# Kernel tuning notes

Measured on AMD Instinct MI355X. Metric: run time of the kernel, lower is better.

## Reference

```python
import jax, jax.numpy as jnp
import numpy as np

B, S, N_STATE, N_HEAD = 2, 2048, 1024, 16
HEAD_DIM = N_STATE // N_HEAD


def setup_inputs() -> dict:
    key = jax.random.key(0)
    ks = jax.random.split(key, 9)
    w_scale = N_STATE ** -0.5
    x = jax.random.normal(ks[0], (B, S, N_STATE), jnp.float32)
    # Whisper-style additive causal mask with -inf above the diagonal
    mask = jnp.triu(jnp.full((S, S), -jnp.inf, jnp.float32), k=1)
    Wq = jax.random.normal(ks[1], (N_STATE, N_STATE), jnp.float32) * w_scale
    bq = jax.random.normal(ks[2], (N_STATE,), jnp.float32) * 0.01
    Wk = jax.random.normal(ks[3], (N_STATE, N_STATE), jnp.float32) * w_scale  # no bias
    Wv = jax.random.normal(ks[4], (N_STATE, N_STATE), jnp.float32) * w_scale
    bv = jax.random.normal(ks[5], (N_STATE,), jnp.float32) * 0.01
    Wo = jax.random.normal(ks[6], (N_STATE, N_STATE), jnp.float32) * w_scale
    bo = jax.random.normal(ks[7], (N_STATE,), jnp.float32) * 0.01
    return {"x": x, "mask": mask, "Wq": Wq, "bq": bq, "Wk": Wk,
            "Wv": Wv, "bv": bv, "Wo": Wo, "bo": bo}


def reference(x, mask, Wq, bq, Wk, Wv, bv, Wo, bo):
    b, s, n_state = x.shape
    scale = (n_state // N_HEAD) ** -0.25
    q = (x @ Wq + bq).reshape(b, s, N_HEAD, HEAD_DIM)  # [b,s,h,d]
    k = (x @ Wk).reshape(b, s, N_HEAD, HEAD_DIM)
    v = (x @ Wv + bv).reshape(b, s, N_HEAD, HEAD_DIM)
    # scale applied to both q and k as in source
    qk = jnp.einsum('bqhd,bkhd->bhqk', q * scale, k * scale)
    qk = qk + mask[:s, :s]
    qk = qk.astype(jnp.float32)
    qk = jnp.where(jnp.isinf(qk), -1e9, qk)
    w = jax.nn.softmax(qk, axis=-1).astype(q.dtype)  # [b,h,q,k]
    wv = jnp.einsum('bhqk,bkhd->bqhd', w, v).reshape(b, s, n_state)
    out = wv @ Wo + bo
    return (out, qk)
```

## Files before the change

kernel.cpp:

```cpp
#include <hip/hip_runtime.h>

typedef __attribute__((ext_vector_type(8))) short short8;
typedef __attribute__((ext_vector_type(4))) float f32x4;

#define SEQ   2048
#define NST   1024
#define NHD   16
#define HDM   64
#define BSZ   2
#define MTOT  (BSZ*SEQ)

__device__ __forceinline__ unsigned short f2bf(float f) {
    union { float f; unsigned int u; } v; v.f = f;
    return (unsigned short)((v.u + 0x7fffu + ((v.u >> 16) & 1u)) >> 16);
}

__device__ __forceinline__ void gload_lds16(const void* g, void* l) {
    __builtin_amdgcn_global_load_lds((const __attribute__((address_space(1))) void*)g,
                                     (__attribute__((address_space(3))) void*)l, 16, 0, 0);
}

__global__ void k_convert(const float* __restrict__ x, unsigned short* __restrict__ out, int n) {
    int i = (blockIdx.x * 256 + threadIdx.x) * 8;
    if (i >= n) return;
    float4 a = *(const float4*)(x + i);
    float4 b = *(const float4*)(x + i + 4);
    short8 v;
    v[0] = (short)f2bf(a.x); v[1] = (short)f2bf(a.y);
    v[2] = (short)f2bf(a.z); v[3] = (short)f2bf(a.w);
    v[4] = (short)f2bf(b.x); v[5] = (short)f2bf(b.y);
    v[6] = (short)f2bf(b.z); v[7] = (short)f2bf(b.w);
    *(short8*)(out + i) = v;
}

__global__ void k_transpose_bf16(const float* __restrict__ W, unsigned short* __restrict__ Wt) {
    __shared__ float t[32][33];
    int n0 = blockIdx.x * 32, k0 = blockIdx.y * 32;
    int c = threadIdx.x & 31, rr = threadIdx.x >> 5;
    for (int i = 0; i < 4; i++) {
        int r = i * 8 + rr;
        t[r][c] = W[(k0 + r) * NST + n0 + c];
    }
    __syncthreads();
    for (int i = 0; i < 4; i++) {
        int r = i * 8 + rr;
        Wt[(n0 + r) * NST + k0 + c] = f2bf(t[c][r]);
    }
}

__global__ void k_vt(const unsigned short* __restrict__ v, unsigned short* __restrict__ vt) {
    __shared__ unsigned short t[64 * 72];
    int jt = blockIdx.x, bh = blockIdx.y;
    int b = bh >> 4, h = bh & 15;
    int tid = threadIdx.x;
    for (int i = 0; i < 2; i++) {
        int id = i * 256 + tid;
        int row = id >> 3, dc = (id & 7) * 8;
        *(short8*)(t + row * 72 + dc) =
            *(const short8*)(v + ((size_t)(b * SEQ + jt * 64 + row)) * NST + h * HDM + dc);
    }
    __syncthreads();
    for (int i = 0; i < 2; i++) {
        int id = i * 256 + tid;
        int d = id >> 3, jc = (id & 7) * 8;
        short8 vv;
        for (int u = 0; u < 8; u++) vv[u] = (short)t[(jc + u) * 72 + d];
        *(short8*)(vt + ((size_t)(bh * HDM + d)) * SEQ + jt * 64 + jc) = vv;
    }
}

template<bool OUT_BF16>
__global__ __launch_bounds__(256) void k_gemm(const unsigned short* __restrict__ A,
                                              const unsigned short* __restrict__ Bt,
                                              const float* __restrict__ bias, float scale,
                                              void* __restrict__ outp) {
    __shared__ __align__(16) unsigned short As[128 * 32];
    __shared__ __align__(16) unsigned short Bs[64 * 32];
    int m0 = blockIdx.y * 128, n0 = blockIdx.x * 64;
    int tid = threadIdx.x, lane = tid & 63, wave = tid >> 6;
    int quad = lane >> 4, l16 = lane & 15;
    int wm = (wave & 1) * 64, wn = (wave >> 1) * 32;
    int p = lane & 3;
    int sz = (quad ^ ((l16 >> 1) & 3)) * 8;
    f32x4 acc[4][2] = {};
    for (int k0 = 0; k0 < NST; k0 += 32) {
        __syncthreads();
        for (int j = 0; j < 2; j++) {
            int row = wave * 32 + j * 16 + (lane >> 2);
            int qb = (p ^ ((row >> 1) & 3)) * 8;
            gload_lds16(A + (size_t)(m0 + row) * NST + k0 + qb, As + (wave * 32 + j * 16) * 32);
        }
        {
            int row = wave * 16 + (lane >> 2);
            int qb = (p ^ ((row >> 1) & 3)) * 8;
            gload_lds16(Bt + (size_t)(n0 + row) * NST + k0 + qb, Bs + wave * 16 * 32);
        }
        __syncthreads();
        short8 a[4], b[2];
        for (int mi = 0; mi < 4; mi++)
            a[mi] = *(const short8*)(As + (wm + mi * 16 + l16) * 32 + sz);
        for (int ni = 0; ni < 2; ni++)
            b[ni] = *(const short8*)(Bs + (wn + ni * 16 + l16) * 32 + sz);
        for (int mi = 0; mi < 4; mi++)
            for (int ni = 0; ni < 2; ni++)
                acc[mi][ni] = __builtin_amdgcn_mfma_f32_16x16x32_bf16(a[mi], b[ni], acc[mi][ni], 0, 0, 0);
    }
    for (int ni = 0; ni < 2; ni++) {
        int col = n0 + wn + ni * 16 + l16;
        float bv = bias ? bias[col] : 0.0f;
        for (int mi = 0; mi < 4; mi++) {
            for (int r = 0; r < 4; r++) {
                int row = m0 + wm + mi * 16 + quad * 4 + r;
                float val = (acc[mi][ni][r] + bv) * scale;
                if (OUT_BF16) ((unsigned short*)outp)[row * NST + col] = f2bf(val);
                else          ((float*)outp)[row * NST + col] = val;
            }
        }
    }
}

__global__ void k_fill_upper(float* __restrict__ qk) {
    int jt = blockIdx.x, qt = blockIdx.y, bh = blockIdx.z;
    if (jt <= qt) return;
    float4 val = make_float4(-1e9f, -1e9f, -1e9f, -1e9f);
    for (int i = 0; i < 4; i++) {
        int lin = i * 256 + threadIdx.x;
        int row = lin >> 4, c4 = (lin & 15) * 4;
        *(float4*)(qk + ((size_t)bh * SEQ + qt * 64 + row) * SEQ + jt * 64 + c4) = val;
    }
}

__global__ __launch_bounds__(256) void k_attn(const unsigned short* __restrict__ qb,
                                              const unsigned short* __restrict__ kb,
                                              const unsigned short* __restrict__ vtg,
                                              float* __restrict__ qk,
                                              unsigned short* __restrict__ wv) {
    __shared__ __align__(16) unsigned short Ks[64 * 64];
    __shared__ __align__(16) unsigned short Vs[64 * 64];
    __shared__ __align__(16) unsigned short Plds[4 * 16 * 72];
    int pair = blockIdx.x, bh = blockIdx.y;
    int b = bh >> 4, h = bh & 15;
    int tid = threadIdx.x, lane = tid & 63, wave = tid >> 6;
    int quad = lane >> 4, l16 = lane & 15;
    unsigned short* pbuf = Plds + wave * 16 * 72;
    int srow = lane >> 3;
    int spb = lane & 7;
    short o1 = (short)0x3F80;
    short8 vones = {o1, o1, o1, o1, o1, o1, o1, o1};
    int fx0 = (quad ^ (l16 & 7)) * 8;
    int fx1 = ((quad + 4) ^ (l16 & 7)) * 8;

    for (int phase = 0; phase < 2; ++phase) {
        int qt = phase ? (31 - pair) : pair;
        int qrow = qt * 64 + wave * 16;
        const unsigned short* qp = qb + ((size_t)(b * SEQ + qrow + l16)) * NST + h * HDM + quad * 8;
        short8 aq0 = *(const short8*)qp;
        short8 aq1 = *(const short8*)(qp + 32);
        f32x4 o[4] = {};
        f32x4 lac = {};

        for (int jt = 0; jt <= qt; jt++) {
            int j0 = jt * 64;
            __syncthreads();
            for (int j = 0; j < 2; j++) {
                int row = wave * 16 + j * 8 + srow;
                int lb = (spb ^ (row & 7)) * 8;
                gload_lds16(kb + ((size_t)(b * SEQ + j0 + row)) * NST + h * HDM + lb,
                            Ks + (wave * 16 + j * 8) * 64);
                gload_lds16(vtg + ((size_t)(bh * HDM + row)) * SEQ + j0 + lb,
                            Vs + (wave * 16 + j * 8) * 64);
            }
            __syncthreads();

            f32x4 s[4];
            for (int c = 0; c < 4; c++) {
                int base = (c * 16 + l16) * 64;
                short8 b0 = *(const short8*)(Ks + base + fx0);
                short8 b1 = *(const short8*)(Ks + base + fx1);
                f32x4 z = {};
                z = __builtin_amdgcn_mfma_f32_16x16x32_bf16(aq0, b0, z, 0, 0, 0);
                s[c] = __builtin_amdgcn_mfma_f32_16x16x32_bf16(aq1, b1, z, 0, 0, 0);
            }

            bool diag = (jt == qt);
            for (int r = 0; r < 4; r++) {
                int i_g = qrow + quad * 4 + r;
                float* qrow_ptr = qk + ((size_t)bh * SEQ + i_g) * SEQ + j0;
                for (int c = 0; c < 4; c++) {
                    int jc = c * 16 + l16;
                    float val = s[c][r];
                    if (diag && (j0 + jc > i_g)) val = -1e9f;
                    qrow_ptr[jc] = val;
                    float pe = __expf(val - 16.0f);
                    pbuf[(quad * 4 + r) * 72 + jc] = f2bf(pe);
                }
            }
            short8 ap0 = *(const short8*)(pbuf + l16 * 72 + quad * 8);
            short8 ap1 = *(const short8*)(pbuf + l16 * 72 + 32 + quad * 8);
            for (int db = 0; db < 4; db++) {
                int base = (db * 16 + l16) * 64;
                short8 b0 = *(const short8*)(Vs + base + fx0);
                short8 b1 = *(const short8*)(Vs + base + fx1);
                o[db] = __builtin_amdgcn_mfma_f32_16x16x32_bf16(ap0, b0, o[db], 0, 0, 0);
                o[db] = __builtin_amdgcn_mfma_f32_16x16x32_bf16(ap1, b1, o[db], 0, 0, 0);
            }
            lac = __builtin_amdgcn_mfma_f32_16x16x32_bf16(ap0, vones, lac, 0, 0, 0);
            lac = __builtin_amdgcn_mfma_f32_16x16x32_bf16(ap1, vones, lac, 0, 0, 0);
        }

        for (int db = 0; db < 4; db++) {
            for (int r = 0; r < 4; r++) {
                int row = qrow + quad * 4 + r;
                wv[((size_t)(b * SEQ + row)) * NST + h * HDM + db * 16 + l16] = f2bf(o[db][r] / lac[r]);
            }
        }
    }
}

extern "C" void kernel_launch(void* const* d_in, const int* in_sizes, int n_in,
                              void* d_out, int out_size, void* d_ws, size_t ws_size,
                              hipStream_t stream) {
    (void)in_sizes; (void)n_in; (void)out_size; (void)ws_size;
    const float* x  = (const float*)d_in[0];
    const float* Wq = (const float*)d_in[2];
    const float* bq = (const float*)d_in[3];
    const float* Wk = (const float*)d_in[4];
    const float* Wv = (const float*)d_in[5];
    const float* bv = (const float*)d_in[6];
    const float* Wo = (const float*)d_in[7];
    const float* bo = (const float*)d_in[8];

    float* out_f  = (float*)d_out;
    float* qk_out = out_f + (size_t)MTOT * NST;

    unsigned short* ws = (unsigned short*)d_ws;
    unsigned short* xb   = ws;
    unsigned short* wqt  = ws + (size_t)4 * 1024 * 1024;
    unsigned short* wkt  = ws + (size_t)5 * 1024 * 1024;
    unsigned short* wvt  = ws + (size_t)6 * 1024 * 1024;
    unsigned short* wot  = ws + (size_t)7 * 1024 * 1024;
    unsigned short* qbuf = ws + (size_t)8  * 1024 * 1024;
    unsigned short* kbuf = ws + (size_t)12 * 1024 * 1024;
    unsigned short* vbuf = ws + (size_t)16 * 1024 * 1024;
    unsigned short* vtb  = ws + (size_t)20 * 1024 * 1024;
    unsigned short* wvb  = xb;

    const float scale = 0.3535533905932738f;

    k_convert<<<2048, 256, 0, stream>>>(x, xb, MTOT * NST);
    dim3 tg(32, 32);
    k_transpose_bf16<<<tg, 256, 0, stream>>>(Wq, wqt);
    k_transpose_bf16<<<tg, 256, 0, stream>>>(Wk, wkt);
    k_transpose_bf16<<<tg, 256, 0, stream>>>(Wv, wvt);
    k_transpose_bf16<<<tg, 256, 0, stream>>>(Wo, wot);

    dim3 gg(16, 32);
    k_gemm<true><<<gg, 256, 0, stream>>>(xb, wqt, bq, scale, qbuf);
    k_gemm<true><<<gg, 256, 0, stream>>>(xb, wkt, nullptr, scale, kbuf);
    k_gemm<true><<<gg, 256, 0, stream>>>(xb, wvt, bv, 1.0f, vbuf);

    k_vt<<<dim3(32, 32), 256, 0, stream>>>(vbuf, vtb);
    k_fill_upper<<<dim3(32, 32, 32), 256, 0, stream>>>(qk_out);
    k_attn<<<dim3(16, 32), 256, 0, stream>>>(qbuf, kbuf, vtb, qk_out, wvb);

    k_gemm<false><<<gg, 256, 0, stream>>>(wvb, wot, bo, 1.0f, (void*)out_f);
}
```

Before: 745.1 us.

## Fuse QKV projections, batch weight transposes, double-buffer attention, fold mask fill

The four weight transposes become one launch, and the Q/K/V projections become a single GEMM over a concatenated N=3072 with a 128x128 tile and a K-step of 64. The attention kernel double-buffers its K/V LDS tiles to overlap loads with compute and writes qk with nontemporal stores. The separate upper-triangle fill kernel is removed and its -1e9 fill moves into the attention epilogue. These changes cut launch count and improve GEMM reuse and attention latency hiding, at the cost of more LDS per block and a heavier attention tail.

```diff
diff --git a/kernel.cpp b/kernel.cpp
--- a/kernel.cpp
+++ b/kernel.cpp
@@ -33,8 +33,12 @@
     *(short8*)(out + i) = v;
 }
 
-__global__ void k_transpose_bf16(const float* __restrict__ W, unsigned short* __restrict__ Wt) {
+__global__ void k_transpose4(const float* __restrict__ W0, const float* __restrict__ W1,
+                             const float* __restrict__ W2, const float* __restrict__ W3,
+                             unsigned short* __restrict__ Wt) {
     __shared__ float t[32][33];
+    const float* W = (blockIdx.z == 0) ? W0 : (blockIdx.z == 1) ? W1 : (blockIdx.z == 2) ? W2 : W3;
+    unsigned short* dst = Wt + ((size_t)blockIdx.z << 20);
     int n0 = blockIdx.x * 32, k0 = blockIdx.y * 32;
     int c = threadIdx.x & 31, rr = threadIdx.x >> 5;
     for (int i = 0; i < 4; i++) {
@@ -44,7 +48,7 @@
     __syncthreads();
     for (int i = 0; i < 4; i++) {
         int r = i * 8 + rr;
-        Wt[(n0 + r) * NST + k0 + c] = f2bf(t[c][r]);
+        dst[(n0 + r) * NST + k0 + c] = f2bf(t[c][r]);
     }
 }
 
@@ -69,64 +73,70 @@
     }
 }
 
-template<bool OUT_BF16>
-__global__ __launch_bounds__(256) void k_gemm(const unsigned short* __restrict__ A,
-                                              const unsigned short* __restrict__ Bt,
-                                              const float* __restrict__ bias, float scale,
-                                              void* __restrict__ outp) {
-    __shared__ __align__(16) unsigned short As[128 * 32];
-    __shared__ __align__(16) unsigned short Bs[64 * 32];
-    int m0 = blockIdx.y * 128, n0 = blockIdx.x * 64;
+template<int MODE>
+__global__ __launch_bounds__(256) void k_gemm128(const unsigned short* __restrict__ A,
+                                                 const unsigned short* __restrict__ Bt,
+                                                 const float* __restrict__ bias0,
+                                                 const float* __restrict__ bias2,
+                                                 float scale, void* __restrict__ outp) {
+    constexpr int BN = (MODE == 1) ? 128 : 64;
+    constexpr int NI = BN / 32;
+    __shared__ __align__(16) unsigned short As[128 * 64];
+    __shared__ __align__(16) unsigned short Bs[BN * 64];
+    int m0 = blockIdx.y * 128, n0 = blockIdx.x * BN;
     int tid = threadIdx.x, lane = tid & 63, wave = tid >> 6;
     int quad = lane >> 4, l16 = lane & 15;
-    int wm = (wave & 1) * 64, wn = (wave >> 1) * 32;
-    int p = lane & 3;
-    int sz = (quad ^ ((l16 >> 1) & 3)) * 8;
-    f32x4 acc[4][2] = {};
-    for (int k0 = 0; k0 < NST; k0 += 32) {
+    int wm = (wave & 1) * 64, wn = (wave >> 1) * (BN / 2);
+    int srow = lane >> 3, spb = lane & 7;
+    f32x4 acc[4][NI] = {};
+    for (int k0 = 0; k0 < NST; k0 += 64) {
         __syncthreads();
-        for (int j = 0; j < 2; j++) {
-            int row = wave * 32 + j * 16 + (lane >> 2);
-            int qb = (p ^ ((row >> 1) & 3)) * 8;
-            gload_lds16(A + (size_t)(m0 + row) * NST + k0 + qb, As + (wave * 32 + j * 16) * 32);
-        }
-        {
-            int row = wave * 16 + (lane >> 2);
-            int qb = (p ^ ((row >> 1) & 3)) * 8;
-            gload_lds16(Bt + (size_t)(n0 + row) * NST + k0 + qb, Bs + wave * 16 * 32);
+        for (int j = 0; j < 4; j++) {
+            int row = wave * 32 + j * 8 + srow;
+            int blk = (spb ^ (row & 7)) * 8;
+            gload_lds16(A + (size_t)(m0 + row) * NST + k0 + blk, As + (wave * 32 + j * 8) * 64);
+        }
+        for (int j = 0; j < NI; j++) {
+            int row = wave * (8 * NI) + j * 8 + srow;
+            int blk = (spb ^ (row & 7)) * 8;
+            gload_lds16(Bt + (size_t)(n0 + row) * NST + k0 + blk, Bs + (wave * 8 * NI + j * 8) * 64);
         }
         __syncthreads();
-        short8 a[4], b[2];
-        for (int mi = 0; mi < 4; mi++)
-            a[mi] = *(const short8*)(As + (wm + mi * 16 + l16) * 32 + sz);
-        for (int ni = 0; ni < 2; ni++)
-            b[ni] = *(const short8*)(Bs + (wn + ni * 16 + l16) * 32 + sz);
-        for (int mi = 0; mi < 4; mi++)
-            for (int ni = 0; ni < 2; ni++)
-                acc[mi][ni] = __builtin_amdgcn_mfma_f32_16x16x32_bf16(a[mi], b[ni], acc[mi][ni], 0, 0, 0);
-    }
-    for (int ni = 0; ni < 2; ni++) {
-        int col = n0 + wn + ni * 16 + l16;
-        float bv = bias ? bias[col] : 0.0f;
-        for (int mi = 0; mi < 4; mi++) {
-            for (int r = 0; r < 4; r++) {
-                int row = m0 + wm + mi * 16 + quad * 4 + r;
-                float val = (acc[mi][ni][r] + bv) * scale;
-                if (OUT_BF16) ((unsigned short*)outp)[row * NST + col] = f2bf(val);
-                else          ((float*)outp)[row * NST + col] = val;
-            }
-        }
-    }
-}
-
-__global__ void k_fill_upper(float* __restrict__ qk) {
-    int jt = blockIdx.x, qt = blockIdx.y, bh = blockIdx.z;
-    if (jt <= qt) return;
-    float4 val = make_float4(-1e9f, -1e9f, -1e9f, -1e9f);
-    for (int i = 0; i < 4; i++) {
-        int lin = i * 256 + threadIdx.x;
-        int row = lin >> 4, c4 = (lin & 15) * 4;
-        *(float4*)(qk + ((size_t)bh * SEQ + qt * 64 + row) * SEQ + jt * 64 + c4) = val;
+        for (int ks = 0; ks < 2; ks++) {
+            short8 a[4], b[NI];
+            for (int mi = 0; mi < 4; mi++) {
+                int r = wm + mi * 16 + l16;
+                a[mi] = *(const short8*)(As + r * 64 + (((ks * 4 + quad) ^ (r & 7)) * 8));
+            }
+            for (int ni = 0; ni < NI; ni++) {
+                int r = wn + ni * 16 + l16;
+                b[ni] = *(const short8*)(Bs + r * 64 + (((ks * 4 + quad) ^ (r & 7)) * 8));
+            }
+            for (int mi = 0; mi < 4; mi++)
+                for (int ni = 0; ni < NI; ni++)
+                    acc[mi][ni] = __builtin_amdgcn_mfma_f32_16x16x32_bf16(a[mi], b[ni], acc[mi][ni], 0, 0, 0);
+        }
+    }
+    for (int ni = 0; ni < NI; ni++) {
+        int ncol = n0 + wn + ni * 16 + l16;
+        if (MODE == 1) {
+            int mat = ncol >> 10, c = ncol & 1023;
+            float bs = (mat == 0) ? bias0[c] : (mat == 2 ? bias2[c] : 0.0f);
+            float sc = (mat == 2) ? 1.0f : scale;
+            unsigned short* dst = (unsigned short*)outp + ((size_t)mat << 22) + c;
+            for (int mi = 0; mi < 4; mi++)
+                for (int r = 0; r < 4; r++) {
+                    int row = m0 + wm + mi * 16 + quad * 4 + r;
+                    dst[(size_t)row * NST] = f2bf((acc[mi][ni][r] + bs) * sc);
+                }
+        } else {
+            float bs = bias0[ncol];
+            for (int mi = 0; mi < 4; mi++)
+                for (int r = 0; r < 4; r++) {
+                    int row = m0 + wm + mi * 16 + quad * 4 + r;
+                    ((float*)outp)[(size_t)row * NST + ncol] = acc[mi][ni][r] + bs;
+                }
+        }
     }
 }
 
@@ -135,8 +145,8 @@
                                               const unsigned short* __restrict__ vtg,
                                               float* __restrict__ qk,
                                               unsigned short* __restrict__ wv) {
-    __shared__ __align__(16) unsigned short Ks[64 * 64];
-    __shared__ __align__(16) unsigned short Vs[64 * 64];
+    __shared__ __align__(16) unsigned short Ks[2][64 * 64];
+    __shared__ __align__(16) unsigned short Vs[2][64 * 64];
     __shared__ __align__(16) unsigned short Plds[4 * 16 * 72];
     int pair = blockIdx.x, bh = blockIdx.y;
     int b = bh >> 4, h = bh & 15;
@@ -149,6 +159,7 @@
     short8 vones = {o1, o1, o1, o1, o1, o1, o1, o1};
     int fx0 = (quad ^ (l16 & 7)) * 8;
     int fx1 = ((quad + 4) ^ (l16 & 7)) * 8;
+    int cur = 0;
 
     for (int phase = 0; phase < 2; ++phase) {
         int qt = phase ? (31 - pair) : pair;
@@ -159,24 +170,38 @@
         f32x4 o[4] = {};
         f32x4 lac = {};
 
+        __syncthreads();
+        for (int j = 0; j < 2; j++) {
+            int row = wave * 16 + j * 8 + srow;
+            int lb = (spb ^ (row & 7)) * 8;
+            gload_lds16(kb + ((size_t)(b * SEQ + row)) * NST + h * HDM + lb,
+                        Ks[cur] + (wave * 16 + j * 8) * 64);
+            gload_lds16(vtg + ((size_t)(bh * HDM + row)) * SEQ + lb,
+                        Vs[cur] + (wave * 16 + j * 8) * 64);
+        }
+
         for (int jt = 0; jt <= qt; jt++) {
             int j0 = jt * 64;
             __syncthreads();
-            for (int j = 0; j < 2; j++) {
-                int row = wave * 16 + j * 8 + srow;
-                int lb = (spb ^ (row & 7)) * 8;
-                gload_lds16(kb + ((size_t)(b * SEQ + j0 + row)) * NST + h * HDM + lb,
-                            Ks + (wave * 16 + j * 8) * 64);
-                gload_lds16(vtg + ((size_t)(bh * HDM + row)) * SEQ + j0 + lb,
-                            Vs + (wave * 16 + j * 8) * 64);
-            }
-            __syncthreads();
+            if (jt < qt) {
+                int jn = j0 + 64;
+                for (int j = 0; j < 2; j++) {
+                    int row = wave * 16 + j * 8 + srow;
+                    int lb = (spb ^ (row & 7)) * 8;
+                    gload_lds16(kb + ((size_t)(b * SEQ + jn + row)) * NST + h * HDM + lb,
+                                Ks[cur ^ 1] + (wave * 16 + j * 8) * 64);
+                    gload_lds16(vtg + ((size_t)(bh * HDM + row)) * SEQ + jn + lb,
+                                Vs[cur ^ 1] + (wave * 16 + j * 8) * 64);
+                }
+            }
+            const unsigned short* KsC = Ks[cur];
+            const unsigned short* VsC = Vs[cur];
 
             f32x4 s[4];
             for (int c = 0; c < 4; c++) {
                 int base = (c * 16 + l16) * 64;
-                short8 b0 = *(const short8*)(Ks + base + fx0);
-                short8 b1 = *(const short8*)(Ks + base + fx1);
+                short8 b0 = *(const short8*)(KsC + base + fx0);
+                short8 b1 = *(const short8*)(KsC + base + fx1);
                 f32x4 z = {};
                 z = __builtin_amdgcn_mfma_f32_16x16x32_bf16(aq0, b0, z, 0, 0, 0);
                 s[c] = __builtin_amdgcn_mfma_f32_16x16x32_bf16(aq1, b1, z, 0, 0, 0);
@@ -190,7 +215,7 @@
                     int jc = c * 16 + l16;
                     float val = s[c][r];
                     if (diag && (j0 + jc > i_g)) val = -1e9f;
-                    qrow_ptr[jc] = val;
+                    __builtin_nontemporal_store(val, qrow_ptr + jc);
                     float pe = __expf(val - 16.0f);
                     pbuf[(quad * 4 + r) * 72 + jc] = f2bf(pe);
                 }
@@ -199,13 +224,14 @@
             short8 ap1 = *(const short8*)(pbuf + l16 * 72 + 32 + quad * 8);
             for (int db = 0; db < 4; db++) {
                 int base = (db * 16 + l16) * 64;
-                short8 b0 = *(const short8*)(Vs + base + fx0);
-                short8 b1 = *(const short8*)(Vs + base + fx1);
+                short8 b0 = *(const short8*)(VsC + base + fx0);
+                short8 b1 = *(const short8*)(VsC + base + fx1);
                 o[db] = __builtin_amdgcn_mfma_f32_16x16x32_bf16(ap0, b0, o[db], 0, 0, 0);
                 o[db] = __builtin_amdgcn_mfma_f32_16x16x32_bf16(ap1, b1, o[db], 0, 0, 0);
             }
             lac = __builtin_amdgcn_mfma_f32_16x16x32_bf16(ap0, vones, lac, 0, 0, 0);
             lac = __builtin_amdgcn_mfma_f32_16x16x32_bf16(ap1, vones, lac, 0, 0, 0);
+            cur ^= 1;
         }
 
         for (int db = 0; db < 4; db++) {
@@ -213,6 +239,14 @@
                 int row = qrow + quad * 4 + r;
                 wv[((size_t)(b * SEQ + row)) * NST + h * HDM + db * 16 + l16] = f2bf(o[db][r] / lac[r]);
             }
+        }
+
+        f32x4 neg = {-1e9f, -1e9f, -1e9f, -1e9f};
+        int c0 = (qt + 1) * 64;
+        for (int r = 0; r < 16; r++) {
+            float* rp = qk + ((size_t)bh * SEQ + qrow + r) * SEQ;
+            for (int c = c0 + lane * 4; c < SEQ; c += 256)
+                __builtin_nontemporal_store(neg, (f32x4*)(rp + c));
         }
     }
 }
@@ -236,8 +270,6 @@
     unsigned short* ws = (unsigned short*)d_ws;
     unsigned short* xb   = ws;
     unsigned short* wqt  = ws + (size_t)4 * 1024 * 1024;
-    unsigned short* wkt  = ws + (size_t)5 * 1024 * 1024;
-    unsigned short* wvt  = ws + (size_t)6 * 1024 * 1024;
     unsigned short* wot  = ws + (size_t)7 * 1024 * 1024;
     unsigned short* qbuf = ws + (size_t)8  * 1024 * 1024;
     unsigned short* kbuf = ws + (size_t)12 * 1024 * 1024;
@@ -248,20 +280,12 @@
     const float scale = 0.3535533905932738f;
 
     k_convert<<<2048, 256, 0, stream>>>(x, xb, MTOT * NST);
-    dim3 tg(32, 32);
-    k_transpose_bf16<<<tg, 256, 0, stream>>>(Wq, wqt);
-    k_transpose_bf16<<<tg, 256, 0, stream>>>(Wk, wkt);
-    k_transpose_bf16<<<tg, 256, 0, stream>>>(Wv, wvt);
-    k_transpose_bf16<<<tg, 256, 0, stream>>>(Wo, wot);
-
-    dim3 gg(16, 32);
-    k_gemm<true><<<gg, 256, 0, stream>>>(xb, wqt, bq, scale, qbuf);
-    k_gemm<true><<<gg, 256, 0, stream>>>(xb, wkt, nullptr, scale, kbuf);
-    k_gemm<true><<<gg, 256, 0, stream>>>(xb, wvt, bv, 1.0f, vbuf);
+    k_transpose4<<<dim3(32, 32, 4), 256, 0, stream>>>(Wq, Wk, Wv, Wo, wqt);
+
+    k_gemm128<1><<<dim3(24, 32), 256, 0, stream>>>(xb, wqt, bq, bv, scale, qbuf);
 
     k_vt<<<dim3(32, 32), 256, 0, stream>>>(vbuf, vtb);
-    k_fill_upper<<<dim3(32, 32, 32), 256, 0, stream>>>(qk_out);
     k_attn<<<dim3(16, 32), 256, 0, stream>>>(qbuf, kbuf, vtb, qk_out, wvb);
 
-    k_gemm<false><<<gg, 256, 0, stream>>>(wvb, wot, bo, 1.0f, (void*)out_f);
-}
+    k_gemm128<0><<<dim3(16, 32), 256, 0, stream>>>(wvb, wot, bo, nullptr, 1.0f, (void*)out_f);
+}
```

Measured after the change: 721.6 us. -3.2%, faster.
